# Optimization experiments

Hardware: AMD Instinct MI355X
Metric: run time of the kernel (lower is better)

Reference implementation:

```python
import jax, jax.numpy as jnp
import numpy as np

N_EMBD = 1024
N_HEAD = 16
HEAD_DIM = N_EMBD // N_HEAD


def setup_inputs() -> dict:
    key = jax.random.key(0)
    kx, kq, kk, kv, ko = jax.random.split(key, 5)
    B, T, C = 2, 2048, N_EMBD
    s = 1.0 / np.sqrt(C)
    return {
        "x": jax.random.normal(kx, (B, T, C), dtype=jnp.float32),
        "Wq": jax.random.normal(kq, (C, C), dtype=jnp.float32) * s,
        "Wk": jax.random.normal(kk, (C, C), dtype=jnp.float32) * s,
        "Wv": jax.random.normal(kv, (C, C), dtype=jnp.float32) * s,
        "Wo": jax.random.normal(ko, (C, C), dtype=jnp.float32) * s,
    }


def reference(x, Wq, Wk, Wv, Wo):
    B, T, C = x.shape
    H, D = N_HEAD, HEAD_DIM
    # projections (torch Linear: y = x @ W^T)
    q = (x @ Wq.T).reshape(B, T, H, D).transpose(0, 2, 1, 3)  # [B,H,T,D]
    k = (x @ Wk.T).reshape(B, T, H, D).transpose(0, 2, 1, 3)
    v = (x @ Wv.T).reshape(B, T, H, D).transpose(0, 2, 1, 3)
    scale = 1.0 / np.sqrt(D).astype(np.float32)
    scores = jnp.einsum("bhqd,bhkd->bhqk", q, k) * scale  # [B,H,T,T]
    causal = jnp.tril(jnp.ones((T, T), dtype=bool))
    scores = jnp.where(causal, scores, -jnp.inf)
    attn = jax.nn.softmax(scores, axis=-1)
    y = jnp.einsum("bhqk,bhkd->bhqd", attn, v)  # [B,H,T,D]
    y = y.transpose(0, 2, 1, 3).reshape(B, T, C)
    return y @ Wo.T
```

## Files before the change

kernel.cpp:

```cpp
#include <hip/hip_runtime.h>
#include <hip/hip_bf16.h>
#include <math.h>

#define SEQ   2048
#define CDIM  1024
#define NH    16
#define HD    64

typedef __attribute__((ext_vector_type(8))) short bf16x8;
typedef __attribute__((ext_vector_type(4))) float f32x4;
typedef __attribute__((ext_vector_type(4))) short short4v;

__device__ __forceinline__ short f2bf(float f) {
  return (short)__builtin_bit_cast(unsigned short, __float2bfloat16(f));
}

__device__ __forceinline__ void glds16(const short* g, short* l) {
  __builtin_amdgcn_global_load_lds(
      (const __attribute__((address_space(1))) unsigned int*)g,
      (__attribute__((address_space(3))) unsigned int*)l, 16, 0, 0);
}

__global__ void cvt_kernel(const float* __restrict__ src, short* __restrict__ dst, int n4) {
  int i = blockIdx.x * blockDim.x + threadIdx.x;
  if (i >= n4) return;
  float4 v = reinterpret_cast<const float4*>(src)[i];
  short4v o;
  o.x = f2bf(v.x); o.y = f2bf(v.y); o.z = f2bf(v.z); o.w = f2bf(v.w);
  reinterpret_cast<short4v*>(dst)[i] = o;
}

template<int MODE>
__global__ __launch_bounds__(256)
void gemm_bt(const short* __restrict__ A,
             const short* __restrict__ W0, const short* __restrict__ W1, const short* __restrict__ W2,
             short* __restrict__ ob0, short* __restrict__ ob1, short* __restrict__ ob2,
             float* __restrict__ of)
{
  constexpr int K = CDIM;
  const int z = (MODE == 0) ? blockIdx.z : 0;
  const short* W;
  short* outb = nullptr;
  if (MODE == 0) {
    W    = (z == 0) ? W0  : (z == 1) ? W1  : W2;
    outb = (z == 0) ? ob0 : (z == 1) ? ob1 : ob2;
  } else {
    W = W0;
  }
  const int m0 = blockIdx.y * 128;
  const int n0 = blockIdx.x * 128;

  __shared__ __align__(16) short As[128 * 32];
  __shared__ __align__(16) short Bs[128 * 32];

  const int tid  = threadIdx.x;
  const int lane = tid & 63;
  const int wid  = tid >> 6;
  const int wr   = wid >> 1;
  const int wc   = wid & 1;
  const int rl   = lane & 15;
  const int g    = lane >> 4;

  f32x4 acc[4][4];
#pragma unroll
  for (int i = 0; i < 4; ++i)
#pragma unroll
    for (int j = 0; j < 4; ++j)
      acc[i][j] = (f32x4){0.f, 0.f, 0.f, 0.f};

  const int lrow = lane >> 2;
  const int lcol = (lane & 3) * 8;
  const int arow = wid * 32 + lrow;

  for (int kt = 0; kt < K / 32; ++kt) {
    const int k0 = kt * 32;
    glds16(&A[(size_t)(m0 + arow) * K + k0 + lcol],      &As[(wid * 32) * 32]);
    glds16(&A[(size_t)(m0 + arow + 16) * K + k0 + lcol], &As[(wid * 32 + 16) * 32]);
    glds16(&W[(size_t)(n0 + arow) * K + k0 + lcol],      &Bs[(wid * 32) * 32]);
    glds16(&W[(size_t)(n0 + arow + 16) * K + k0 + lcol], &Bs[(wid * 32 + 16) * 32]);
    __syncthreads();

    bf16x8 af[4], bfr[4];
#pragma unroll
    for (int mi = 0; mi < 4; ++mi)
      af[mi] = *(const bf16x8*)&As[(wr * 64 + mi * 16 + rl) * 32 + g * 8];
#pragma unroll
    for (int nj = 0; nj < 4; ++nj)
      bfr[nj] = *(const bf16x8*)&Bs[(wc * 64 + nj * 16 + rl) * 32 + g * 8];
#pragma unroll
    for (int mi = 0; mi < 4; ++mi)
#pragma unroll
      for (int nj = 0; nj < 4; ++nj)
        acc[mi][nj] = __builtin_amdgcn_mfma_f32_16x16x32_bf16(af[mi], bfr[nj], acc[mi][nj], 0, 0, 0);
    __syncthreads();
  }

#pragma unroll
  for (int mi = 0; mi < 4; ++mi) {
#pragma unroll
    for (int nj = 0; nj < 4; ++nj) {
      const int gmb = m0 + wr * 64 + mi * 16 + g * 4;
      const int gn  = n0 + wc * 64 + nj * 16 + rl;
      if (MODE == 0 && z == 2) {
        short4v pk;
#pragma unroll
        for (int r = 0; r < 4; ++r) pk[r] = f2bf(acc[mi][nj][r]);
        const int b = gmb >> 11, t = gmb & 2047;
        const int h = gn >> 6,  d = gn & 63;
        *(short4v*)&outb[(((size_t)(b * NH + h)) * HD + d) * SEQ + t] = pk;
      } else {
#pragma unroll
        for (int r = 0; r < 4; ++r) {
          const int gm = gmb + r;
          const float val = acc[mi][nj][r];
          if (MODE == 0) {
            const int b = gm >> 11, t = gm & 2047;
            const int h = gn >> 6,  d = gn & 63;
            outb[(((size_t)(b * NH + h)) * SEQ + t) * HD + d] = f2bf(val);
          } else {
            of[(size_t)gm * CDIM + gn] = val;
          }
        }
      }
    }
  }
}

__global__ __launch_bounds__(256)
void attn_kernel(const short* __restrict__ q, const short* __restrict__ k,
                 const short* __restrict__ vt, short* __restrict__ yb)
{
  const int bh  = blockIdx.y;
  const int pp  = blockIdx.x;
  const int jA  = pp;
  const int jB  = 31 - pp;
  const int tid = threadIdx.x;
  const int lane = tid & 63;
  const int wid  = tid >> 6;
  const int rl   = lane & 15;
  const int g    = lane >> 4;

  const short* Qp = q  + (size_t)bh * SEQ * HD;
  const short* Kp = k  + (size_t)bh * SEQ * HD;
  const short* Vp = vt + (size_t)bh * HD * SEQ;

  __shared__ short Ks[64 * 72];
  __shared__ short Vs[64 * 72];
  __shared__ short Ps[4][2][16 * 72];

  const int q0A = jA * 64 + wid * 16;
  const int q0B = jB * 64 + wid * 16;

  bf16x8 qfA[2], qfB[2];
#pragma unroll
  for (int ds = 0; ds < 2; ++ds) {
    qfA[ds] = *(const bf16x8*)&Qp[(size_t)(q0A + rl) * HD + ds * 32 + g * 8];
    qfB[ds] = *(const bf16x8*)&Qp[(size_t)(q0B + rl) * HD + ds * 32 + g * 8];
  }

  f32x4 accA[4], accB[4];
  float mA[4], lA[4], mB[4], lB[4];
#pragma unroll
  for (int r = 0; r < 4; ++r) { mA[r] = -INFINITY; lA[r] = 0.f; mB[r] = -INFINITY; lB[r] = 0.f; }
#pragma unroll
  for (int nt = 0; nt < 4; ++nt) { accA[nt] = (f32x4){0,0,0,0}; accB[nt] = (f32x4){0,0,0,0}; }

  const float scale = 0.125f;
  const int srow = tid >> 3;
  const int scol = (tid & 7) * 8;

  auto process = [&](bf16x8 (&qf)[2], f32x4 (&acc)[4], float (&m_run)[4], float (&l_run)[4],
                     bool diag, short* PsW) {
    f32x4 s_[4];
#pragma unroll
    for (int ct = 0; ct < 4; ++ct) s_[ct] = (f32x4){0, 0, 0, 0};
    __builtin_amdgcn_s_setprio(1);
#pragma unroll
    for (int ct = 0; ct < 4; ++ct)
#pragma unroll
      for (int ds = 0; ds < 2; ++ds) {
        bf16x8 kf = *(const bf16x8*)&Ks[(ct * 16 + rl) * 72 + ds * 32 + g * 8];
        s_[ct] = __builtin_amdgcn_mfma_f32_16x16x32_bf16(qf[ds], kf, s_[ct], 0, 0, 0);
      }
    __builtin_amdgcn_s_setprio(0);

    float pm[4] = {-INFINITY, -INFINITY, -INFINITY, -INFINITY};
#pragma unroll
    for (int ct = 0; ct < 4; ++ct)
#pragma unroll
      for (int r = 0; r < 4; ++r) {
        float sv = s_[ct][r] * scale;
        if (diag) {
          const int lq = wid * 16 + g * 4 + r;
          const int lk = ct * 16 + rl;
          sv = (lk <= lq) ? sv : -INFINITY;
        }
        s_[ct][r] = sv;
        pm[r] = fmaxf(pm[r], sv);
      }

    bool need = false;
#pragma unroll
    for (int r = 0; r < 4; ++r) need = need || (pm[r] > m_run[r]);
    if (__any((int)need)) {
#pragma unroll
      for (int r = 0; r < 4; ++r) {
        pm[r] = fmaxf(pm[r], __shfl_xor(pm[r], 1));
        pm[r] = fmaxf(pm[r], __shfl_xor(pm[r], 2));
        pm[r] = fmaxf(pm[r], __shfl_xor(pm[r], 4));
        pm[r] = fmaxf(pm[r], __shfl_xor(pm[r], 8));
        const float mnew = fmaxf(m_run[r], pm[r]);
        const float f = __expf(m_run[r] - mnew);
        m_run[r] = mnew;
        l_run[r] *= f;
#pragma unroll
        for (int nt = 0; nt < 4; ++nt) acc[nt][r] *= f;
      }
    }

#pragma unroll
    for (int ct = 0; ct < 4; ++ct) {
      const int c = ct * 16 + rl;
#pragma unroll
      for (int r = 0; r < 4; ++r) {
        const float p = __expf(s_[ct][r] - m_run[r]);
        l_run[r] += p;
        PsW[(g * 4 + r) * 72 + c] = f2bf(p);
      }
    }

    __builtin_amdgcn_s_setprio(1);
#pragma unroll
    for (int ks = 0; ks < 2; ++ks) {
      bf16x8 pf = *(const bf16x8*)&PsW[rl * 72 + ks * 32 + g * 8];
#pragma unroll
      for (int nt = 0; nt < 4; ++nt) {
        bf16x8 vf = *(const bf16x8*)&Vs[(nt * 16 + rl) * 72 + ks * 32 + g * 8];
        acc[nt] = __builtin_amdgcn_mfma_f32_16x16x32_bf16(pf, vf, acc[nt], 0, 0, 0);
      }
    }
    __builtin_amdgcn_s_setprio(0);
  };

  auto epilogue = [&](f32x4 (&acc)[4], float (&l_run)[4], int q0w) {
    const int b = bh >> 4, h = bh & 15;
#pragma unroll
    for (int r = 0; r < 4; ++r) {
      float lr = l_run[r];
      lr += __shfl_xor(lr, 1);
      lr += __shfl_xor(lr, 2);
      lr += __shfl_xor(lr, 4);
      lr += __shfl_xor(lr, 8);
      const float inv = 1.0f / lr;
      const int qq = q0w + g * 4 + r;
#pragma unroll
      for (int nt = 0; nt < 4; ++nt)
        yb[((size_t)b * SEQ + qq) * CDIM + h * HD + nt * 16 + rl] = f2bf(acc[nt][r] * inv);
    }
  };

  bf16x8 k0 = *(const bf16x8*)&Kp[(size_t)srow * HD + scol];
  bf16x8 k1 = *(const bf16x8*)&Kp[(size_t)(srow + 32) * HD + scol];
  bf16x8 v0 = *(const bf16x8*)&Vp[(size_t)srow * SEQ + scol];
  bf16x8 v1 = *(const bf16x8*)&Vp[(size_t)(srow + 32) * SEQ + scol];

  for (int t = 0; t <= jB; ++t) {
    __syncthreads();
    *(bf16x8*)&Ks[srow * 72 + scol]        = k0;
    *(bf16x8*)&Ks[(srow + 32) * 72 + scol] = k1;
    *(bf16x8*)&Vs[srow * 72 + scol]        = v0;
    *(bf16x8*)&Vs[(srow + 32) * 72 + scol] = v1;
    __syncthreads();

    if (t < jB) {
      const int kn = (t + 1) * 64;
      k0 = *(const bf16x8*)&Kp[(size_t)(kn + srow) * HD + scol];
      k1 = *(const bf16x8*)&Kp[(size_t)(kn + srow + 32) * HD + scol];
      v0 = *(const bf16x8*)&Vp[(size_t)srow * SEQ + kn + scol];
      v1 = *(const bf16x8*)&Vp[(size_t)(srow + 32) * SEQ + kn + scol];
    }

    process(qfB, accB, mB, lB, t == jB, &Ps[wid][0][0]);
    if (t <= jA)
      process(qfA, accA, mA, lA, t == jA, &Ps[wid][1][0]);
  }

  epilogue(accB, lB, q0B);
  epilogue(accA, lA, q0A);
}

extern "C" void kernel_launch(void* const* d_in, const int* in_sizes, int n_in,
                              void* d_out, int out_size, void* d_ws, size_t ws_size,
                              hipStream_t stream) {
  const float* x  = (const float*)d_in[0];
  const float* Wq = (const float*)d_in[1];
  const float* Wk = (const float*)d_in[2];
  const float* Wv = (const float*)d_in[3];
  const float* Wo = (const float*)d_in[4];
  float* out = (float*)d_out;

  char* ws = (char*)d_ws;
  short* xb  = (short*)(ws);
  short* Wqb = (short*)(ws + ((size_t)8  << 20));
  short* Wkb = (short*)(ws + ((size_t)10 << 20));
  short* Wvb = (short*)(ws + ((size_t)12 << 20));
  short* Wob = (short*)(ws + ((size_t)14 << 20));
  short* qb  = (short*)(ws + ((size_t)16 << 20));
  short* kbp = (short*)(ws + ((size_t)24 << 20));
  short* vtp = (short*)(ws + ((size_t)32 << 20));
  short* yb  = (short*)(ws + ((size_t)40 << 20));

  cvt_kernel<<<4096, 256, 0, stream>>>(x,  xb,  1048576);
  cvt_kernel<<<1024, 256, 0, stream>>>(Wq, Wqb, 262144);
  cvt_kernel<<<1024, 256, 0, stream>>>(Wk, Wkb, 262144);
  cvt_kernel<<<1024, 256, 0, stream>>>(Wv, Wvb, 262144);
  cvt_kernel<<<1024, 256, 0, stream>>>(Wo, Wob, 262144);

  gemm_bt<0><<<dim3(8, 32, 3), 256, 0, stream>>>(xb, Wqb, Wkb, Wvb, qb, kbp, vtp, nullptr);

  attn_kernel<<<dim3(16, 32), 256, 0, stream>>>(qb, kbp, vtp, yb);

  gemm_bt<1><<<dim3(8, 32, 1), 256, 0, stream>>>(yb, Wob, nullptr, nullptr,
                                                 nullptr, nullptr, nullptr, out);
}
```

Before: 137.8 us.

## Fold softmax scale into Wk, use exp2, merge weight casts, narrow output GEMM tile

The softmax scale times log2(e) is folded into Wk during its bf16 conversion, so the attention kernel drops the per-score multiply and uses exp2f instead of __expf. The four weight conversions are merged into one launch. The output projection GEMM uses a 64-wide N tile, giving 512 blocks instead of 256 so more CUs are busy. The causal mask now compares absolute key and query indices. Folding the scale into Wk before rounding to bf16 slightly changes numerics.

```diff
diff --git a/kernel.cpp b/kernel.cpp
--- a/kernel.cpp
+++ b/kernel.cpp
@@ -6,6 +6,8 @@
 #define CDIM  1024
 #define NH    16
 #define HD    64
+
+#define K_SCALE 0.1803368801111204f
 
 typedef __attribute__((ext_vector_type(8))) short bf16x8;
 typedef __attribute__((ext_vector_type(4))) float f32x4;
@@ -30,7 +32,23 @@
   reinterpret_cast<short4v*>(dst)[i] = o;
 }
 
-template<int MODE>
+__global__ void cvtw_kernel(const float* __restrict__ w0, const float* __restrict__ w1,
+                            const float* __restrict__ w2, const float* __restrict__ w3,
+                            short* __restrict__ d0, short* __restrict__ d1,
+                            short* __restrict__ d2, short* __restrict__ d3) {
+  const int y = blockIdx.y;
+  const float* src = (y == 0) ? w0 : (y == 1) ? w1 : (y == 2) ? w2 : w3;
+  short* dst       = (y == 0) ? d0 : (y == 1) ? d1 : (y == 2) ? d2 : d3;
+  const float mult = (y == 1) ? K_SCALE : 1.0f;
+  int i = blockIdx.x * blockDim.x + threadIdx.x;
+  float4 v = reinterpret_cast<const float4*>(src)[i];
+  short4v o;
+  o.x = f2bf(v.x * mult); o.y = f2bf(v.y * mult);
+  o.z = f2bf(v.z * mult); o.w = f2bf(v.w * mult);
+  reinterpret_cast<short4v*>(dst)[i] = o;
+}
+
+template<int MODE, int BN>
 __global__ __launch_bounds__(256)
 void gemm_bt(const short* __restrict__ A,
              const short* __restrict__ W0, const short* __restrict__ W1, const short* __restrict__ W2,
@@ -38,6 +56,7 @@
              float* __restrict__ of)
 {
   constexpr int K = CDIM;
+  constexpr int NJF = BN / 32;
   const int z = (MODE == 0) ? blockIdx.z : 0;
   const short* W;
   short* outb = nullptr;
@@ -48,10 +67,10 @@
     W = W0;
   }
   const int m0 = blockIdx.y * 128;
-  const int n0 = blockIdx.x * 128;
+  const int n0 = blockIdx.x * BN;
 
   __shared__ __align__(16) short As[128 * 32];
-  __shared__ __align__(16) short Bs[128 * 32];
+  __shared__ __align__(16) short Bs[BN * 32];
 
   const int tid  = threadIdx.x;
   const int lane = tid & 63;
@@ -61,11 +80,11 @@
   const int rl   = lane & 15;
   const int g    = lane >> 4;
 
-  f32x4 acc[4][4];
+  f32x4 acc[4][NJF];
 #pragma unroll
   for (int i = 0; i < 4; ++i)
 #pragma unroll
-    for (int j = 0; j < 4; ++j)
+    for (int j = 0; j < NJF; ++j)
       acc[i][j] = (f32x4){0.f, 0.f, 0.f, 0.f};
 
   const int lrow = lane >> 2;
@@ -76,21 +95,25 @@
     const int k0 = kt * 32;
     glds16(&A[(size_t)(m0 + arow) * K + k0 + lcol],      &As[(wid * 32) * 32]);
     glds16(&A[(size_t)(m0 + arow + 16) * K + k0 + lcol], &As[(wid * 32 + 16) * 32]);
-    glds16(&W[(size_t)(n0 + arow) * K + k0 + lcol],      &Bs[(wid * 32) * 32]);
-    glds16(&W[(size_t)(n0 + arow + 16) * K + k0 + lcol], &Bs[(wid * 32 + 16) * 32]);
+    if constexpr (BN == 128) {
+      glds16(&W[(size_t)(n0 + arow) * K + k0 + lcol],      &Bs[(wid * 32) * 32]);
+      glds16(&W[(size_t)(n0 + arow + 16) * K + k0 + lcol], &Bs[(wid * 32 + 16) * 32]);
+    } else {
+      glds16(&W[(size_t)(n0 + wid * 16 + lrow) * K + k0 + lcol], &Bs[(wid * 16) * 32]);
+    }
     __syncthreads();
 
-    bf16x8 af[4], bfr[4];
+    bf16x8 af[4], bfr[NJF];
 #pragma unroll
     for (int mi = 0; mi < 4; ++mi)
       af[mi] = *(const bf16x8*)&As[(wr * 64 + mi * 16 + rl) * 32 + g * 8];
 #pragma unroll
-    for (int nj = 0; nj < 4; ++nj)
-      bfr[nj] = *(const bf16x8*)&Bs[(wc * 64 + nj * 16 + rl) * 32 + g * 8];
+    for (int nj = 0; nj < NJF; ++nj)
+      bfr[nj] = *(const bf16x8*)&Bs[(wc * (BN / 2) + nj * 16 + rl) * 32 + g * 8];
 #pragma unroll
     for (int mi = 0; mi < 4; ++mi)
 #pragma unroll
-      for (int nj = 0; nj < 4; ++nj)
+      for (int nj = 0; nj < NJF; ++nj)
         acc[mi][nj] = __builtin_amdgcn_mfma_f32_16x16x32_bf16(af[mi], bfr[nj], acc[mi][nj], 0, 0, 0);
     __syncthreads();
   }
@@ -98,9 +121,9 @@
 #pragma unroll
   for (int mi = 0; mi < 4; ++mi) {
 #pragma unroll
-    for (int nj = 0; nj < 4; ++nj) {
+    for (int nj = 0; nj < NJF; ++nj) {
       const int gmb = m0 + wr * 64 + mi * 16 + g * 4;
-      const int gn  = n0 + wc * 64 + nj * 16 + rl;
+      const int gn  = n0 + wc * (BN / 2) + nj * 16 + rl;
       if (MODE == 0 && z == 2) {
         short4v pk;
 #pragma unroll
@@ -165,12 +188,11 @@
 #pragma unroll
   for (int nt = 0; nt < 4; ++nt) { accA[nt] = (f32x4){0,0,0,0}; accB[nt] = (f32x4){0,0,0,0}; }
 
-  const float scale = 0.125f;
   const int srow = tid >> 3;
   const int scol = (tid & 7) * 8;
 
   auto process = [&](bf16x8 (&qf)[2], f32x4 (&acc)[4], float (&m_run)[4], float (&l_run)[4],
-                     bool diag, short* PsW) {
+                     bool diag, int t, int q0w, short* PsW) {
     f32x4 s_[4];
 #pragma unroll
     for (int ct = 0; ct < 4; ++ct) s_[ct] = (f32x4){0, 0, 0, 0};
@@ -189,11 +211,11 @@
     for (int ct = 0; ct < 4; ++ct)
 #pragma unroll
       for (int r = 0; r < 4; ++r) {
-        float sv = s_[ct][r] * scale;
+        float sv = s_[ct][r];
         if (diag) {
-          const int lq = wid * 16 + g * 4 + r;
-          const int lk = ct * 16 + rl;
-          sv = (lk <= lq) ? sv : -INFINITY;
+          const int key = t * 64 + ct * 16 + rl;
+          const int qq  = q0w + g * 4 + r;
+          sv = (key <= qq) ? sv : -INFINITY;
         }
         s_[ct][r] = sv;
         pm[r] = fmaxf(pm[r], sv);
@@ -210,7 +232,7 @@
         pm[r] = fmaxf(pm[r], __shfl_xor(pm[r], 4));
         pm[r] = fmaxf(pm[r], __shfl_xor(pm[r], 8));
         const float mnew = fmaxf(m_run[r], pm[r]);
-        const float f = __expf(m_run[r] - mnew);
+        const float f = exp2f(m_run[r] - mnew);
         m_run[r] = mnew;
         l_run[r] *= f;
 #pragma unroll
@@ -223,7 +245,7 @@
       const int c = ct * 16 + rl;
 #pragma unroll
       for (int r = 0; r < 4; ++r) {
-        const float p = __expf(s_[ct][r] - m_run[r]);
+        const float p = exp2f(s_[ct][r] - m_run[r]);
         l_run[r] += p;
         PsW[(g * 4 + r) * 72 + c] = f2bf(p);
       }
@@ -280,9 +302,9 @@
       v1 = *(const bf16x8*)&Vp[(size_t)(srow + 32) * SEQ + kn + scol];
     }
 
-    process(qfB, accB, mB, lB, t == jB, &Ps[wid][0][0]);
+    process(qfB, accB, mB, lB, t == jB, t, q0B, &Ps[wid][0][0]);
     if (t <= jA)
-      process(qfA, accA, mA, lA, t == jA, &Ps[wid][1][0]);
+      process(qfA, accA, mA, lA, t == jA, t, q0A, &Ps[wid][1][0]);
   }
 
   epilogue(accB, lB, q0B);
@@ -310,16 +332,13 @@
   short* vtp = (short*)(ws + ((size_t)32 << 20));
   short* yb  = (short*)(ws + ((size_t)40 << 20));
 
-  cvt_kernel<<<4096, 256, 0, stream>>>(x,  xb,  1048576);
-  cvt_kernel<<<1024, 256, 0, stream>>>(Wq, Wqb, 262144);
-  cvt_kernel<<<1024, 256, 0, stream>>>(Wk, Wkb, 262144);
-  cvt_kernel<<<1024, 256, 0, stream>>>(Wv, Wvb, 262144);
-  cvt_kernel<<<1024, 256, 0, stream>>>(Wo, Wob, 262144);
-
-  gemm_bt<0><<<dim3(8, 32, 3), 256, 0, stream>>>(xb, Wqb, Wkb, Wvb, qb, kbp, vtp, nullptr);
+  cvt_kernel<<<4096, 256, 0, stream>>>(x, xb, 1048576);
+  cvtw_kernel<<<dim3(1024, 4), 256, 0, stream>>>(Wq, Wk, Wv, Wo, Wqb, Wkb, Wvb, Wob);
+
+  gemm_bt<0, 128><<<dim3(8, 32, 3), 256, 0, stream>>>(xb, Wqb, Wkb, Wvb, qb, kbp, vtp, nullptr);
 
   attn_kernel<<<dim3(16, 32), 256, 0, stream>>>(qb, kbp, vtp, yb);
 
-  gemm_bt<1><<<dim3(8, 32, 1), 256, 0, stream>>>(yb, Wob, nullptr, nullptr,
-                                                 nullptr, nullptr, nullptr, out);
-}
+  gemm_bt<1, 64><<<dim3(16, 32, 1), 256, 0, stream>>>(yb, Wob, nullptr, nullptr,
+                                                      nullptr, nullptr, nullptr, out);
+}
```

After: 135.5 us. About the same (-1.6%).
